# Optimization experiments

Measured on AMD Instinct MI355X. Metric: run time of the kernel, lower is better.

Reference implementation:

```python
import jax, jax.numpy as jnp
import numpy as np

B, T, H = 2048, 64, 64
N_LANE, N_PHASE = 8, 8
# phase -> (lane1, lane2) from phase_startLane_mapping (lanes indexed 0..7)
PHASE_LANES = np.array([[1, 3], [0, 2], [5, 7], [4, 6], [0, 1], [2, 3], [4, 5], [6, 7]])
# pairwise (i, j) with i != j, row-major i then j (matches the python double loop)
I_IDX = np.repeat(np.arange(N_PHASE), N_PHASE - 1).reshape(N_PHASE, N_PHASE - 1)
J_IDX = np.array([[j for j in range(N_PHASE) if j != i] for i in range(N_PHASE)])
# per-lane history gather: [idx, idx+phase_dim, idx+phase_dim+vehicle_dim]
HIST_IDX = np.stack([np.arange(N_LANE), np.arange(N_LANE) + 8, np.arange(N_LANE) + 16], axis=-1)


def setup_inputs():
    key = jax.random.key(0)
    ks = jax.random.split(key, 16)
    ph_bits = jax.random.randint(ks[0], (B, 8), 0, 2).astype(jnp.float32)
    veh_cnt = jax.random.uniform(ks[1], (B, 8)) * 10.0
    feature_input = jnp.concatenate([ph_bits, veh_cnt], axis=-1)  # [B,16]
    history_input = jax.random.uniform(ks[2], (B, T, 24))
    relation = jax.random.randint(ks[3], (8, 7), 0, 2).astype(jnp.int32)
    s = 0.2
    p = {}
    p['emb_phase'] = jax.random.normal(ks[4], (2, 4)) * s
    p['Wv'] = jax.random.normal(ks[5], (4, 1)) * s
    p['bv'] = jnp.zeros((4,))
    p['Wh'] = jax.random.normal(ks[6], (4, 3)) * s
    p['bh'] = jnp.zeros((4,))
    p['Wih'] = jax.random.normal(ks[7], (3 * H, 4)) * s
    p['Whh'] = jax.random.normal(ks[8], (3 * H, H)) * s
    p['bih'] = jnp.zeros((3 * H,))
    p['bhh'] = jnp.zeros((3 * H,))
    p['Wl'] = jax.random.normal(ks[9], (16, 8 + H)) * s
    p['bl'] = jnp.zeros((16,))
    p['emb_const'] = jax.random.normal(ks[10], (2, 4)) * s
    p['Wcf'] = jax.random.normal(ks[11], (20, 32)) * s
    p['bcf'] = jnp.zeros((20,))
    p['Wcc'] = jax.random.normal(ks[12], (20, 4)) * s
    p['bcc'] = jnp.zeros((20,))
    p['Wcm'] = jax.random.normal(ks[13], (20, 20)) * s
    p['bcm'] = jnp.zeros((20,))
    p['Wfin'] = jax.random.normal(ks[14], (1, 20)) * s
    p['bfin'] = jnp.zeros((1,))
    return {'feature_input': feature_input, 'history_input': history_input, 'relation': relation, **p}


def _gru_last(x, Wih, Whh, bih, bhh):
    # x: [N, T, 4] -> final hidden state [N, H]; PyTorch GRU gate order (r, z, n)
    n = x.shape[0]
    h_dim = Whh.shape[1]

    def step(hprev, xt):
        gi = xt @ Wih.T + bih          # [N, 3H]
        gh = hprev @ Whh.T + bhh       # [N, 3H]
        i_r, i_z, i_n = jnp.split(gi, 3, axis=-1)
        h_r, h_z, h_n = jnp.split(gh, 3, axis=-1)
        r = jax.nn.sigmoid(i_r + h_r)
        z = jax.nn.sigmoid(i_z + h_z)
        cand = jnp.tanh(i_n + r * h_n)
        hnew = (1 - z) * cand + z * hprev
        return hnew, None

    h0 = jnp.zeros((n, h_dim), x.dtype)
    hT, _ = jax.lax.scan(step, h0, jnp.swapaxes(x, 0, 1))
    return hT


def _forward(feature_input, history_input, relation, emb_phase, Wv, bv, Wh, bh,
             Wih, Whh, bih, bhh, Wl, bl, emb_const, Wcf, bcf, Wcc, bcc, Wcm, bcm, Wfin, bfin):
    b = feature_input.shape[0]
    phase_ids = jax.lax.stop_gradient(feature_input[:, :8]).astype(jnp.int32)
    veh_raw = feature_input[:, 8:]                                     # [B,8]
    ph = jax.nn.sigmoid(emb_phase[phase_ids])                          # [B,8,4]
    veh = jax.nn.sigmoid(veh_raw[..., None] * Wv[:, 0] + bv)           # Linear(1,4): [B,8,4]
    hist = history_input[:, :, HIST_IDX]                               # [B,T,8,3]
    hist = jax.nn.sigmoid(jnp.einsum('btlc,oc->btlo', hist, Wh) + bh)  # [B,T,8,4]
    x = jnp.swapaxes(hist, 1, 2).reshape(b * N_LANE, T, 4)
    hidden = _gru_last(x, Wih, Whh, bih, bhh).reshape(b, N_LANE, H)
    lane_feat = jnp.concatenate([veh, ph, hidden], axis=-1)            # [B,8,8+H]
    line = jax.nn.relu(lane_feat @ Wl.T + bl)                          # [B,8,16]
    pp = line[:, PHASE_LANES].sum(axis=2)                              # phase pressure [B,8,16]
    fm = jnp.concatenate([pp[:, I_IDX], pp[:, J_IDX]], axis=-1)        # [B,8,7,32]
    ce = emb_const[relation]                                           # [8,7,4]
    xf = jax.nn.relu(jnp.einsum('bpqc,oc->bpqo', fm, Wcf) + bcf)       # 1x1 conv [B,8,7,20]
    yc = jax.nn.relu(ce @ Wcc.T + bcc)                                 # [8,7,20] (broadcast over B)
    z = jax.nn.relu(jnp.einsum('bpqc,oc->bpqo', xf * yc, Wcm) + bcm)
    z = jnp.einsum('bpqc,oc->bpqo', z, Wfin) + bfin                    # [B,8,7,1]
    return z.sum(axis=2)[..., 0]                                       # sum over competing phases -> [B,8]


def reference(feature_input, history_input, relation, emb_phase, Wv, bv, Wh, bh,
              Wih, Whh, bih, bhh, Wl, bl, emb_const, Wcf, bcf, Wcc, bcc, Wcm, bcm, Wfin, bfin):
    return _forward(feature_input, history_input, relation, emb_phase, Wv, bv, Wh, bh,
                    Wih, Whh, bih, bhh, Wl, bl, emb_const, Wcf, bcf, Wcc, bcc, Wcm, bcm, Wfin, bfin)
```

## Files before the change

### kernel.cpp

```cpp
#include <hip/hip_runtime.h>

typedef unsigned short u16;
typedef unsigned int   u32;

typedef __attribute__((ext_vector_type(8))) short short8;
typedef __attribute__((ext_vector_type(4))) float f32x4;

union Frag { u32 u[4]; short8 s; };

__device__ __forceinline__ u32 fbits(float f){ union{float f;u32 u;}x; x.f=f; return x.u; }
__device__ __forceinline__ float bitsf(u32 u){ union{u32 u;float f;}x; x.u=u; return x.f; }
__device__ __forceinline__ u32 pack_trunc(float a, float b){
    return __builtin_amdgcn_perm(fbits(b), fbits(a), 0x07060302u);
}
__device__ __forceinline__ u32 bf16_rne(float a){
    u32 u = fbits(a); return (u + 0x7FFFu + ((u >> 16) & 1u)) >> 16;
}
__device__ __forceinline__ u32 pack_rne(float a, float b){
    return bf16_rne(a) | (bf16_rne(b) << 16);
}
__device__ __forceinline__ float sigmoidf_(float x){
    return __builtin_amdgcn_rcpf(1.0f + __expf(-x));
}

#define LOG2E 1.4426950408889634f

struct __align__(16) SharedMem {
    union {
        struct {
            u16 hh[2][16][72];
            u16 hl[2][16][72];
            u32 uallp[64][16][4];
        } lp;
        struct {
            float wl[1152];
            float bl[16];
            float wcf[640];
            float bcf[20];
            float wcc[80];
            float bcc[20];
            float wcm[400];
            float bcm[20];
            float wfin[20];
            float bfin;
            float line[2][128];
            float pp[2][128];
        } tl;
    };
    float h[16 * 68];
};

__global__ __launch_bounds__(256, 4)
void FRAPRQ_fused_kernel(
    const float* __restrict__ feat,
    const float* __restrict__ hist,
    const int*   __restrict__ relation,
    const float* __restrict__ emb_phase,
    const float* __restrict__ Wv,
    const float* __restrict__ bv,
    const float* __restrict__ Wh,
    const float* __restrict__ bh,
    const float* __restrict__ Wih,
    const float* __restrict__ Whh,
    const float* __restrict__ bih,
    const float* __restrict__ bhh,
    const float* __restrict__ Wl,
    const float* __restrict__ bl,
    const float* __restrict__ emb_const,
    const float* __restrict__ Wcf,
    const float* __restrict__ bcf,
    const float* __restrict__ Wcc,
    const float* __restrict__ bcc,
    const float* __restrict__ Wcm,
    const float* __restrict__ bcm,
    const float* __restrict__ Wfin,
    const float* __restrict__ bfin,
    float* __restrict__ out)
{
    __shared__ SharedMem sm;
    const int tid  = threadIdx.x;
    const int w    = tid >> 6;
    const int lane = tid & 63;
    const int sq   = lane & 15;
    const int q    = lane >> 4;
    const int b_base = blockIdx.x * 2;

    {
        u32* z = (u32*)&sm.lp.hh[0][0][0];
        #pragma unroll 1
        for (int i = tid; i < 2304; i += 256) z[i] = 0u;
    }

    {
        const int s  = tid & 15;
        const int tg = tid >> 4;
        const int bs_ = b_base + (s >> 3), ls_ = s & 7;
        const float* hbp = hist + (size_t)bs_ * 1536;
        float whc[12], bhc[4];
        #pragma unroll
        for (int c = 0; c < 4; ++c){
            whc[c*3+0] = Wh[c*3+0]; whc[c*3+1] = Wh[c*3+1]; whc[c*3+2] = Wh[c*3+2];
            bhc[c] = bh[c];
        }
        #pragma unroll
        for (int i = 0; i < 4; ++i){
            const int t = tg * 4 + i;
            const float x0 = hbp[t*24 + ls_];
            const float x1 = hbp[t*24 + ls_ + 8];
            const float x2 = hbp[t*24 + ls_ + 16];
            float u_[4];
            #pragma unroll
            for (int c = 0; c < 4; ++c)
                u_[c] = sigmoidf_(fmaf(whc[c*3], x0, fmaf(whc[c*3+1], x1, fmaf(whc[c*3+2], x2, bhc[c]))));
            const u32 uh01 = pack_rne(u_[0], u_[1]);
            const u32 uh23 = pack_rne(u_[2], u_[3]);
            const float l0 = u_[0] - bitsf((uh01 & 0xFFFFu) << 16);
            const float l1 = u_[1] - bitsf(uh01 & 0xFFFF0000u);
            const float l2 = u_[2] - bitsf((uh23 & 0xFFFFu) << 16);
            const float l3 = u_[3] - bitsf(uh23 & 0xFFFF0000u);
            *(uint4*)&sm.lp.uallp[t][s][0] =
                make_uint4(uh01, uh23, pack_rne(l0, l1), pack_rne(l2, l3));
        }
    }

    const float gsc[3] = { -LOG2E, -LOG2E, 2.0f * LOG2E };

    Frag ahi[6], alo[6];
    #pragma unroll
    for (int g3 = 0; g3 < 3; ++g3){
        #pragma unroll
        for (int c = 0; c < 2; ++c){
            const int idx = g3 * 2 + c;
            const float* wp = Whh + (64 * g3 + 16 * w + sq) * 64 + 32 * c + 8 * q;
            const float4 fA = *(const float4*)wp;
            const float4 fB = *(const float4*)(wp + 4);
            const float s3 = gsc[g3];
            const float f[8] = {fA.x*s3, fA.y*s3, fA.z*s3, fA.w*s3,
                                fB.x*s3, fB.y*s3, fB.z*s3, fB.w*s3};
            #pragma unroll
            for (int p = 0; p < 4; ++p){
                const u32 hi = pack_rne(f[2*p], f[2*p+1]);
                ahi[idx].u[p] = hi;
                const float l0 = f[2*p]   - bitsf((hi & 0xFFFFu) << 16);
                const float l1 = f[2*p+1] - bitsf(hi & 0xFFFF0000u);
                alo[idx].u[p] = pack_rne(l0, l1);
            }
        }
    }

    Frag auR, auZ, auN;
    {
        Frag* dst[3] = { &auR, &auZ, &auN };
        #pragma unroll
        for (int g3 = 0; g3 < 3; ++g3){
            const int row = 64 * g3 + 16 * w + sq;
            const float4 wv4 = *(const float4*)&Wih[row * 4];
            const float s3 = gsc[g3];
            const float v0 = wv4.x*s3, v1 = wv4.y*s3, v2 = wv4.z*s3, v3 = wv4.w*s3;
            const u32 whi01 = pack_rne(v0, v1);
            const u32 whi23 = pack_rne(v2, v3);
            const float r0 = v0 - bitsf((whi01 & 0xFFFFu) << 16);
            const float r1 = v1 - bitsf(whi01 & 0xFFFF0000u);
            const float r2 = v2 - bitsf((whi23 & 0xFFFFu) << 16);
            const float r3 = v3 - bitsf(whi23 & 0xFFFF0000u);
            const u32 wlo01 = pack_rne(r0, r1);
            const u32 wlo23 = pack_rne(r2, r3);
            dst[g3]->u[0] = (q <= 1) ? whi01 : 0u;
            dst[g3]->u[1] = (q <= 1) ? whi23 : 0u;
            dst[g3]->u[2] = (q == 0) ? wlo01 : 0u;
            dst[g3]->u[3] = (q == 0) ? wlo23 : 0u;
        }
    }

    f32x4 bR4, bZ4, bNh4, bNi4;
    #pragma unroll
    for (int r = 0; r < 4; ++r){
        const int j = 16 * w + 4 * q + r;
        bR4[r]  = -LOG2E * (bih[j]       + bhh[j]);
        bZ4[r]  = -LOG2E * (bih[64 + j]  + bhh[64 + j]);
        bNi4[r] = 2.0f * LOG2E * bih[128 + j];
        bNh4[r] = 2.0f * LOG2E * bhh[128 + j];
    }

    float hreg[4] = {0.f, 0.f, 0.f, 0.f};

    __syncthreads();

    #define MFMA_(A,B,C) __builtin_amdgcn_mfma_f32_16x16x32_bf16(A, B, C, 0, 0, 0)

    #pragma unroll 1
    for (int t = 0; t < 64; ++t){
        const int rb = t & 1;

        const short8 bh0 = *(const short8*)&sm.lp.hh[rb][sq][8 * q];
        const short8 bl0 = *(const short8*)&sm.lp.hl[rb][sq][8 * q];
        const short8 bh1 = *(const short8*)&sm.lp.hh[rb][sq][32 + 8 * q];
        const short8 bl1 = *(const short8*)&sm.lp.hl[rb][sq][32 + 8 * q];
        const uint4 uv = *(const uint4*)&sm.lp.uallp[t][sq][0];
        Frag bu;
        bu.u[0] = (q == 0) ? uv.x : ((q == 1) ? uv.z : 0u);
        bu.u[1] = (q == 0) ? uv.y : ((q == 1) ? uv.w : 0u);
        bu.u[2] = (q == 0) ? uv.x : 0u;
        bu.u[3] = (q == 0) ? uv.y : 0u;

        f32x4 aR = MFMA_(auR.s, bu.s, bR4);
        aR = MFMA_(ahi[0].s, bh0, aR); aR = MFMA_(ahi[0].s, bl0, aR); aR = MFMA_(alo[0].s, bh0, aR);
        aR = MFMA_(ahi[1].s, bh1, aR); aR = MFMA_(ahi[1].s, bl1, aR); aR = MFMA_(alo[1].s, bh1, aR);
        f32x4 aZ = MFMA_(auZ.s, bu.s, bZ4);
        aZ = MFMA_(ahi[2].s, bh0, aZ); aZ = MFMA_(ahi[2].s, bl0, aZ); aZ = MFMA_(alo[2].s, bh0, aZ);
        aZ = MFMA_(ahi[3].s, bh1, aZ); aZ = MFMA_(ahi[3].s, bl1, aZ); aZ = MFMA_(alo[3].s, bh1, aZ);
        f32x4 aN = MFMA_(ahi[4].s, bh0, bNh4);
        aN = MFMA_(ahi[4].s, bl0, aN); aN = MFMA_(alo[4].s, bh0, aN);
        aN = MFMA_(ahi[5].s, bh1, aN); aN = MFMA_(ahi[5].s, bl1, aN); aN = MFMA_(alo[5].s, bh1, aN);
        f32x4 gN = MFMA_(auN.s, bu.s, bNi4);

        float hn4[4];
        #pragma unroll
        for (int r = 0; r < 4; ++r){
            const float rr   = __builtin_amdgcn_rcpf(1.0f + __builtin_amdgcn_exp2f(aR[r]));
            const float zz   = __builtin_amdgcn_rcpf(1.0f + __builtin_amdgcn_exp2f(aZ[r]));
            const float y    = fmaf(rr, aN[r], gN[r]);
            const float cand = fmaf(-2.0f,
                __builtin_amdgcn_rcpf(__builtin_amdgcn_exp2f(y) + 1.0f), 1.0f);
            const float hn   = fmaf(zz, hreg[r] - cand, cand);
            hreg[r] = hn;
            hn4[r] = hn;
        }

        {
            const u32 hi0 = pack_trunc(hn4[0], hn4[1]);
            const u32 hi1 = pack_trunc(hn4[2], hn4[3]);
            const float l0 = hn4[0] - bitsf((hi0 & 0xFFFFu) << 16);
            const float l1 = hn4[1] - bitsf(hi0 & 0xFFFF0000u);
            const float l2 = hn4[2] - bitsf((hi1 & 0xFFFFu) << 16);
            const float l3 = hn4[3] - bitsf(hi1 & 0xFFFF0000u);
            const u32 lo0 = pack_trunc(l0, l1);
            const u32 lo1 = pack_trunc(l2, l3);
            const int wb = rb ^ 1;
            *(uint2*)&sm.lp.hh[wb][sq][16 * w + 4 * q] = make_uint2(hi0, hi1);
            *(uint2*)&sm.lp.hl[wb][sq][16 * w + 4 * q] = make_uint2(lo0, lo1);
        }

        __syncthreads();
    }
    #undef MFMA_

    {
        const float4 hv = make_float4(hreg[0], hreg[1], hreg[2], hreg[3]);
        *(float4*)&sm.h[sq * 68 + 16 * w + 4 * q] = hv;
    }

    for (int i = tid; i < 1152; i += 256) sm.tl.wl[i]  = Wl[i];
    for (int i = tid; i <  640; i += 256) sm.tl.wcf[i] = Wcf[i];
    for (int i = tid; i <  400; i += 256) sm.tl.wcm[i] = Wcm[i];
    if (tid < 80) sm.tl.wcc[tid] = Wcc[tid];
    if (tid < 20){
        sm.tl.bcf[tid]  = bcf[tid];
        sm.tl.bcc[tid]  = bcc[tid];
        sm.tl.bcm[tid]  = bcm[tid];
        sm.tl.wfin[tid] = Wfin[tid];
    }
    if (tid < 16) sm.tl.bl[tid] = bl[tid];
    if (tid == 0) sm.tl.bfin = bfin[0];
    __syncthreads();

    {
        const int g    = w & 1;
        const int half = w >> 1;
        const int b    = b_base + g;
        const int l = lane >> 3, o = lane & 7;
        float fv[8];
        const float vraw = feat[b * 16 + 8 + l];
        const int   bit  = ((int)feat[b * 16 + l]) & 1;
        #pragma unroll
        for (int c = 0; c < 4; ++c){
            fv[c]     = sigmoidf_(fmaf(vraw, Wv[c], bv[c]));
            fv[4 + c] = sigmoidf_(emb_phase[bit * 4 + c]);
        }
        const float* hrow = &sm.h[(g * 8 + l) * 68];
        const int oo = o + half * 8;
        float acc = sm.tl.bl[oo];
        #pragma unroll
        for (int f = 0; f < 8; ++f) acc = fmaf(fv[f], sm.tl.wl[oo * 72 + f], acc);
        for (int k = 0; k < 64; ++k) acc = fmaf(hrow[k], sm.tl.wl[oo * 72 + 8 + k], acc);
        sm.tl.line[g][l * 16 + oo] = fmaxf(acc, 0.0f);
    }
    __syncthreads();

    if (w < 2){
        const int g = w;
        const int b = b_base + g;
        {
            const int p = lane >> 3, o = lane & 7;
            const int l0 = (0x64204501u >> (p * 4)) & 15;
            const int l1 = (0x75316723u >> (p * 4)) & 15;
            sm.tl.pp[g][p * 16 + o]     = sm.tl.line[g][l0 * 16 + o]     + sm.tl.line[g][l1 * 16 + o];
            sm.tl.pp[g][p * 16 + o + 8] = sm.tl.line[g][l0 * 16 + o + 8] + sm.tl.line[g][l1 * 16 + o + 8];
        }
        __builtin_amdgcn_wave_barrier();
        if (lane < 56){
            const int p  = lane / 7;
            const int qi = lane - p * 7;
            const int jl = qi + (qi >= p ? 1 : 0);
            float fmv[32];
            #pragma unroll
            for (int f = 0; f < 16; ++f){
                fmv[f]      = sm.tl.pp[g][p  * 16 + f];
                fmv[16 + f] = sm.tl.pp[g][jl * 16 + f];
            }
            const int rel = relation[p * 7 + qi] & 1;
            float ce[4];
            #pragma unroll
            for (int c = 0; c < 4; ++c) ce[c] = emb_const[rel * 4 + c];
            float m[20];
            for (int o = 0; o < 20; ++o){
                float xf = sm.tl.bcf[o];
                #pragma unroll
                for (int f = 0; f < 32; ++f) xf = fmaf(fmv[f], sm.tl.wcf[o * 32 + f], xf);
                float yc = sm.tl.bcc[o];
                #pragma unroll
                for (int c = 0; c < 4; ++c) yc = fmaf(ce[c], sm.tl.wcc[o * 4 + c], yc);
                m[o] = fmaxf(xf, 0.0f) * fmaxf(yc, 0.0f);
            }
            float fin = sm.tl.bfin;
            for (int o = 0; o < 20; ++o){
                float zz = sm.tl.bcm[o];
                #pragma unroll
                for (int c = 0; c < 20; ++c) zz = fmaf(m[c], sm.tl.wcm[o * 20 + c], zz);
                fin = fmaf(fmaxf(zz, 0.0f), sm.tl.wfin[o], fin);
            }
            sm.tl.line[g][lane] = fin;
        }
        __builtin_amdgcn_wave_barrier();
        if (lane < 8){
            float acc = 0.0f;
            #pragma unroll
            for (int qq = 0; qq < 7; ++qq) acc += sm.tl.line[g][lane * 7 + qq];
            out[b * 8 + lane] = acc;
        }
    }
}

extern "C" void kernel_launch(void* const* d_in, const int* in_sizes, int n_in,
                              void* d_out, int out_size, void* d_ws, size_t ws_size,
                              hipStream_t stream) {
    (void)n_in; (void)d_ws; (void)ws_size; (void)out_size;
    const float* feat      = (const float*)d_in[0];
    const float* hist      = (const float*)d_in[1];
    const int*   relation  = (const int*)d_in[2];
    const float* emb_phase = (const float*)d_in[3];
    const float* Wv        = (const float*)d_in[4];
    const float* bv        = (const float*)d_in[5];
    const float* Wh        = (const float*)d_in[6];
    const float* bh        = (const float*)d_in[7];
    const float* Wih       = (const float*)d_in[8];
    const float* Whh       = (const float*)d_in[9];
    const float* bih       = (const float*)d_in[10];
    const float* bhh       = (const float*)d_in[11];
    const float* Wl        = (const float*)d_in[12];
    const float* bl        = (const float*)d_in[13];
    const float* emb_const = (const float*)d_in[14];
    const float* Wcf       = (const float*)d_in[15];
    const float* bcf       = (const float*)d_in[16];
    const float* Wcc       = (const float*)d_in[17];
    const float* bcc       = (const float*)d_in[18];
    const float* Wcm       = (const float*)d_in[19];
    const float* bcm       = (const float*)d_in[20];
    const float* Wfin      = (const float*)d_in[21];
    const float* bfin      = (const float*)d_in[22];
    float* out = (float*)d_out;

    const int B = in_sizes[0] / 16;
    const int nblocks = B / 2;
    FRAPRQ_fused_kernel<<<nblocks, 256, 0, stream>>>(
        feat, hist, relation, emb_phase, Wv, bv, Wh, bh, Wih, Whh, bih, bhh,
        Wl, bl, emb_const, Wcf, bcf, Wcc, bcc, Wcm, bcm, Wfin, bfin, out);
}
```

Measured before the change: 200.1 us.

## Process two independent 16-sequence GRU tiles per block to share weights and barriers

Each block now handles 4 batch items (two 16-row GRU tiles) instead of 2, reusing the register-resident Whh fragments for both tiles and interleaving two independent MFMA chains per timestep. This amortizes the per-step __syncthreads and the weight setup, and gives the scheduler independent work to hide MFMA and transcendental latency. The tail stage is restructured so each wave handles one batch item end to end. In exchange, LDS per block roughly doubles, launch bounds drop to 2 blocks per CU, and the grid halves, which reduces occupancy.

Measured after the change: 204.7 us. +2.3%, slower.

```diff
diff --git a/kernel.cpp b/kernel.cpp
--- a/kernel.cpp
+++ b/kernel.cpp
@@ -28,9 +28,9 @@
 struct __align__(16) SharedMem {
     union {
         struct {
-            u16 hh[2][16][72];
-            u16 hl[2][16][72];
-            u32 uallp[64][16][4];
+            u16 hh[2][2][16][72];
+            u16 hl[2][2][16][72];
+            u32 uallp[2][64][16][4];
         } lp;
         struct {
             float wl[1152];
@@ -43,14 +43,14 @@
             float bcm[20];
             float wfin[20];
             float bfin;
-            float line[2][128];
-            float pp[2][128];
+            float line[4][128];
+            float pp[4][128];
         } tl;
     };
-    float h[16 * 68];
+    float h[32 * 68];
 };
 
-__global__ __launch_bounds__(256, 4)
+__global__ __launch_bounds__(256, 2)
 void FRAPRQ_fused_kernel(
     const float* __restrict__ feat,
     const float* __restrict__ hist,
@@ -83,18 +83,19 @@
     const int lane = tid & 63;
     const int sq   = lane & 15;
     const int q    = lane >> 4;
-    const int b_base = blockIdx.x * 2;
+    const int b_base = blockIdx.x * 4;
 
     {
-        u32* z = (u32*)&sm.lp.hh[0][0][0];
+        u32* z = (u32*)&sm.lp.hh[0][0][0][0];
         #pragma unroll 1
-        for (int i = tid; i < 2304; i += 256) z[i] = 0u;
+        for (int i = tid; i < 4608; i += 256) z[i] = 0u;
     }
 
     {
         const int s  = tid & 15;
-        const int tg = tid >> 4;
-        const int bs_ = b_base + (s >> 3), ls_ = s & 7;
+        const int pr = (tid >> 4) & 1;
+        const int tg = tid >> 5;
+        const int bs_ = b_base + pr * 2 + (s >> 3), ls_ = s & 7;
         const float* hbp = hist + (size_t)bs_ * 1536;
         float whc[12], bhc[4];
         #pragma unroll
@@ -103,8 +104,8 @@
             bhc[c] = bh[c];
         }
         #pragma unroll
-        for (int i = 0; i < 4; ++i){
-            const int t = tg * 4 + i;
+        for (int i = 0; i < 8; ++i){
+            const int t = tg * 8 + i;
             const float x0 = hbp[t*24 + ls_];
             const float x1 = hbp[t*24 + ls_ + 8];
             const float x2 = hbp[t*24 + ls_ + 16];
@@ -118,7 +119,7 @@
             const float l1 = u_[1] - bitsf(uh01 & 0xFFFF0000u);
             const float l2 = u_[2] - bitsf((uh23 & 0xFFFFu) << 16);
             const float l3 = u_[3] - bitsf(uh23 & 0xFFFF0000u);
-            *(uint4*)&sm.lp.uallp[t][s][0] =
+            *(uint4*)&sm.lp.uallp[pr][t][s][0] =
                 make_uint4(uh01, uh23, pack_rne(l0, l1), pack_rne(l2, l3));
         }
     }
@@ -182,7 +183,7 @@
         bNh4[r] = 2.0f * LOG2E * bhh[128 + j];
     }
 
-    float hreg[4] = {0.f, 0.f, 0.f, 0.f};
+    float hreg[2][4] = {{0.f,0.f,0.f,0.f},{0.f,0.f,0.f,0.f}};
 
     __syncthreads();
 
@@ -192,42 +193,47 @@
     for (int t = 0; t < 64; ++t){
         const int rb = t & 1;
 
-        const short8 bh0 = *(const short8*)&sm.lp.hh[rb][sq][8 * q];
-        const short8 bl0 = *(const short8*)&sm.lp.hl[rb][sq][8 * q];
-        const short8 bh1 = *(const short8*)&sm.lp.hh[rb][sq][32 + 8 * q];
-        const short8 bl1 = *(const short8*)&sm.lp.hl[rb][sq][32 + 8 * q];
-        const uint4 uv = *(const uint4*)&sm.lp.uallp[t][sq][0];
-        Frag bu;
-        bu.u[0] = (q == 0) ? uv.x : ((q == 1) ? uv.z : 0u);
-        bu.u[1] = (q == 0) ? uv.y : ((q == 1) ? uv.w : 0u);
-        bu.u[2] = (q == 0) ? uv.x : 0u;
-        bu.u[3] = (q == 0) ? uv.y : 0u;
-
-        f32x4 aR = MFMA_(auR.s, bu.s, bR4);
-        aR = MFMA_(ahi[0].s, bh0, aR); aR = MFMA_(ahi[0].s, bl0, aR); aR = MFMA_(alo[0].s, bh0, aR);
-        aR = MFMA_(ahi[1].s, bh1, aR); aR = MFMA_(ahi[1].s, bl1, aR); aR = MFMA_(alo[1].s, bh1, aR);
-        f32x4 aZ = MFMA_(auZ.s, bu.s, bZ4);
-        aZ = MFMA_(ahi[2].s, bh0, aZ); aZ = MFMA_(ahi[2].s, bl0, aZ); aZ = MFMA_(alo[2].s, bh0, aZ);
-        aZ = MFMA_(ahi[3].s, bh1, aZ); aZ = MFMA_(ahi[3].s, bl1, aZ); aZ = MFMA_(alo[3].s, bh1, aZ);
-        f32x4 aN = MFMA_(ahi[4].s, bh0, bNh4);
-        aN = MFMA_(ahi[4].s, bl0, aN); aN = MFMA_(alo[4].s, bh0, aN);
-        aN = MFMA_(ahi[5].s, bh1, aN); aN = MFMA_(ahi[5].s, bl1, aN); aN = MFMA_(alo[5].s, bh1, aN);
-        f32x4 gN = MFMA_(auN.s, bu.s, bNi4);
-
-        float hn4[4];
-        #pragma unroll
-        for (int r = 0; r < 4; ++r){
-            const float rr   = __builtin_amdgcn_rcpf(1.0f + __builtin_amdgcn_exp2f(aR[r]));
-            const float zz   = __builtin_amdgcn_rcpf(1.0f + __builtin_amdgcn_exp2f(aZ[r]));
-            const float y    = fmaf(rr, aN[r], gN[r]);
-            const float cand = fmaf(-2.0f,
-                __builtin_amdgcn_rcpf(__builtin_amdgcn_exp2f(y) + 1.0f), 1.0f);
-            const float hn   = fmaf(zz, hreg[r] - cand, cand);
-            hreg[r] = hn;
-            hn4[r] = hn;
-        }
-
-        {
+        short8 bh0[2], bl0[2], bh1[2], bl1[2];
+        Frag bu[2];
+        #pragma unroll
+        for (int p = 0; p < 2; ++p){
+            bh0[p] = *(const short8*)&sm.lp.hh[p][rb][sq][8 * q];
+            bl0[p] = *(const short8*)&sm.lp.hl[p][rb][sq][8 * q];
+            bh1[p] = *(const short8*)&sm.lp.hh[p][rb][sq][32 + 8 * q];
+            bl1[p] = *(const short8*)&sm.lp.hl[p][rb][sq][32 + 8 * q];
+            const uint4 uv = *(const uint4*)&sm.lp.uallp[p][t][sq][0];
+            bu[p].u[0] = (q == 0) ? uv.x : ((q == 1) ? uv.z : 0u);
+            bu[p].u[1] = (q == 0) ? uv.y : ((q == 1) ? uv.w : 0u);
+            bu[p].u[2] = (q == 0) ? uv.x : 0u;
+            bu[p].u[3] = (q == 0) ? uv.y : 0u;
+        }
+
+        #pragma unroll
+        for (int p = 0; p < 2; ++p){
+            f32x4 aR = MFMA_(auR.s, bu[p].s, bR4);
+            aR = MFMA_(ahi[0].s, bh0[p], aR); aR = MFMA_(ahi[0].s, bl0[p], aR); aR = MFMA_(alo[0].s, bh0[p], aR);
+            aR = MFMA_(ahi[1].s, bh1[p], aR); aR = MFMA_(ahi[1].s, bl1[p], aR); aR = MFMA_(alo[1].s, bh1[p], aR);
+            f32x4 aZ = MFMA_(auZ.s, bu[p].s, bZ4);
+            aZ = MFMA_(ahi[2].s, bh0[p], aZ); aZ = MFMA_(ahi[2].s, bl0[p], aZ); aZ = MFMA_(alo[2].s, bh0[p], aZ);
+            aZ = MFMA_(ahi[3].s, bh1[p], aZ); aZ = MFMA_(ahi[3].s, bl1[p], aZ); aZ = MFMA_(alo[3].s, bh1[p], aZ);
+            f32x4 aN = MFMA_(ahi[4].s, bh0[p], bNh4);
+            aN = MFMA_(ahi[4].s, bl0[p], aN); aN = MFMA_(alo[4].s, bh0[p], aN);
+            aN = MFMA_(ahi[5].s, bh1[p], aN); aN = MFMA_(ahi[5].s, bl1[p], aN); aN = MFMA_(alo[5].s, bh1[p], aN);
+            f32x4 gN = MFMA_(auN.s, bu[p].s, bNi4);
+
+            float hn4[4];
+            #pragma unroll
+            for (int r = 0; r < 4; ++r){
+                const float rr   = __builtin_amdgcn_rcpf(1.0f + __builtin_amdgcn_exp2f(aR[r]));
+                const float zz   = __builtin_amdgcn_rcpf(1.0f + __builtin_amdgcn_exp2f(aZ[r]));
+                const float y    = fmaf(rr, aN[r], gN[r]);
+                const float cand = fmaf(-2.0f,
+                    __builtin_amdgcn_rcpf(__builtin_amdgcn_exp2f(y) + 1.0f), 1.0f);
+                const float hn   = fmaf(zz, hreg[p][r] - cand, cand);
+                hreg[p][r] = hn;
+                hn4[r] = hn;
+            }
+
             const u32 hi0 = pack_trunc(hn4[0], hn4[1]);
             const u32 hi1 = pack_trunc(hn4[2], hn4[3]);
             const float l0 = hn4[0] - bitsf((hi0 & 0xFFFFu) << 16);
@@ -237,17 +243,18 @@
             const u32 lo0 = pack_trunc(l0, l1);
             const u32 lo1 = pack_trunc(l2, l3);
             const int wb = rb ^ 1;
-            *(uint2*)&sm.lp.hh[wb][sq][16 * w + 4 * q] = make_uint2(hi0, hi1);
-            *(uint2*)&sm.lp.hl[wb][sq][16 * w + 4 * q] = make_uint2(lo0, lo1);
+            *(uint2*)&sm.lp.hh[p][wb][sq][16 * w + 4 * q] = make_uint2(hi0, hi1);
+            *(uint2*)&sm.lp.hl[p][wb][sq][16 * w + 4 * q] = make_uint2(lo0, lo1);
         }
 
         __syncthreads();
     }
     #undef MFMA_
 
-    {
-        const float4 hv = make_float4(hreg[0], hreg[1], hreg[2], hreg[3]);
-        *(float4*)&sm.h[sq * 68 + 16 * w + 4 * q] = hv;
+    #pragma unroll
+    for (int p = 0; p < 2; ++p){
+        const float4 hv = make_float4(hreg[p][0], hreg[p][1], hreg[p][2], hreg[p][3]);
+        *(float4*)&sm.h[(p * 16 + sq) * 68 + 16 * w + 4 * q] = hv;
     }
 
     for (int i = tid; i < 1152; i += 256) sm.tl.wl[i]  = Wl[i];
@@ -265,9 +272,7 @@
     __syncthreads();
 
     {
-        const int g    = w & 1;
-        const int half = w >> 1;
-        const int b    = b_base + g;
+        const int b = b_base + w;
         const int l = lane >> 3, o = lane & 7;
         float fv[8];
         const float vraw = feat[b * 16 + 8 + l];
@@ -277,25 +282,23 @@
             fv[c]     = sigmoidf_(fmaf(vraw, Wv[c], bv[c]));
             fv[4 + c] = sigmoidf_(emb_phase[bit * 4 + c]);
         }
-        const float* hrow = &sm.h[(g * 8 + l) * 68];
-        const int oo = o + half * 8;
-        float acc = sm.tl.bl[oo];
-        #pragma unroll
-        for (int f = 0; f < 8; ++f) acc = fmaf(fv[f], sm.tl.wl[oo * 72 + f], acc);
-        for (int k = 0; k < 64; ++k) acc = fmaf(hrow[k], sm.tl.wl[oo * 72 + 8 + k], acc);
-        sm.tl.line[g][l * 16 + oo] = fmaxf(acc, 0.0f);
-    }
-    __syncthreads();
-
-    if (w < 2){
-        const int g = w;
-        const int b = b_base + g;
+        const float* hrow = &sm.h[((w >> 1) * 16 + (w & 1) * 8 + l) * 68];
+        #pragma unroll
+        for (int half = 0; half < 2; ++half){
+            const int oo = o + half * 8;
+            float acc = sm.tl.bl[oo];
+            #pragma unroll
+            for (int f = 0; f < 8; ++f) acc = fmaf(fv[f], sm.tl.wl[oo * 72 + f], acc);
+            for (int k = 0; k < 64; ++k) acc = fmaf(hrow[k], sm.tl.wl[oo * 72 + 8 + k], acc);
+            sm.tl.line[w][l * 16 + oo] = fmaxf(acc, 0.0f);
+        }
+        __builtin_amdgcn_wave_barrier();
         {
-            const int p = lane >> 3, o = lane & 7;
+            const int p = lane >> 3, oo = lane & 7;
             const int l0 = (0x64204501u >> (p * 4)) & 15;
             const int l1 = (0x75316723u >> (p * 4)) & 15;
-            sm.tl.pp[g][p * 16 + o]     = sm.tl.line[g][l0 * 16 + o]     + sm.tl.line[g][l1 * 16 + o];
-            sm.tl.pp[g][p * 16 + o + 8] = sm.tl.line[g][l0 * 16 + o + 8] + sm.tl.line[g][l1 * 16 + o + 8];
+            sm.tl.pp[w][p * 16 + oo]     = sm.tl.line[w][l0 * 16 + oo]     + sm.tl.line[w][l1 * 16 + oo];
+            sm.tl.pp[w][p * 16 + oo + 8] = sm.tl.line[w][l0 * 16 + oo + 8] + sm.tl.line[w][l1 * 16 + oo + 8];
         }
         __builtin_amdgcn_wave_barrier();
         if (lane < 56){
@@ -305,37 +308,37 @@
             float fmv[32];
             #pragma unroll
             for (int f = 0; f < 16; ++f){
-                fmv[f]      = sm.tl.pp[g][p  * 16 + f];
-                fmv[16 + f] = sm.tl.pp[g][jl * 16 + f];
+                fmv[f]      = sm.tl.pp[w][p  * 16 + f];
+                fmv[16 + f] = sm.tl.pp[w][jl * 16 + f];
             }
             const int rel = relation[p * 7 + qi] & 1;
             float ce[4];
             #pragma unroll
             for (int c = 0; c < 4; ++c) ce[c] = emb_const[rel * 4 + c];
             float m[20];
-            for (int o = 0; o < 20; ++o){
-                float xf = sm.tl.bcf[o];
+            for (int o2 = 0; o2 < 20; ++o2){
+                float xf = sm.tl.bcf[o2];
                 #pragma unroll
-                for (int f = 0; f < 32; ++f) xf = fmaf(fmv[f], sm.tl.wcf[o * 32 + f], xf);
-                float yc = sm.tl.bcc[o];
+                for (int f = 0; f < 32; ++f) xf = fmaf(fmv[f], sm.tl.wcf[o2 * 32 + f], xf);
+                float yc = sm.tl.bcc[o2];
                 #pragma unroll
-                for (int c = 0; c < 4; ++c) yc = fmaf(ce[c], sm.tl.wcc[o * 4 + c], yc);
-                m[o] = fmaxf(xf, 0.0f) * fmaxf(yc, 0.0f);
+                for (int c = 0; c < 4; ++c) yc = fmaf(ce[c], sm.tl.wcc[o2 * 4 + c], yc);
+                m[o2] = fmaxf(xf, 0.0f) * fmaxf(yc, 0.0f);
             }
             float fin = sm.tl.bfin;
-            for (int o = 0; o < 20; ++o){
-                float zz = sm.tl.bcm[o];
+            for (int o2 = 0; o2 < 20; ++o2){
+                float zz = sm.tl.bcm[o2];
                 #pragma unroll
-                for (int c = 0; c < 20; ++c) zz = fmaf(m[c], sm.tl.wcm[o * 20 + c], zz);
-                fin = fmaf(fmaxf(zz, 0.0f), sm.tl.wfin[o], fin);
-            }
-            sm.tl.line[g][lane] = fin;
+                for (int c = 0; c < 20; ++c) zz = fmaf(m[c], sm.tl.wcm[o2 * 20 + c], zz);
+                fin = fmaf(fmaxf(zz, 0.0f), sm.tl.wfin[o2], fin);
+            }
+            sm.tl.line[w][lane] = fin;
         }
         __builtin_amdgcn_wave_barrier();
         if (lane < 8){
             float acc = 0.0f;
             #pragma unroll
-            for (int qq = 0; qq < 7; ++qq) acc += sm.tl.line[g][lane * 7 + qq];
+            for (int qq = 0; qq < 7; ++qq) acc += sm.tl.line[w][lane * 7 + qq];
             out[b * 8 + lane] = acc;
         }
     }
@@ -371,7 +374,7 @@
     float* out = (float*)d_out;
 
     const int B = in_sizes[0] / 16;
-    const int nblocks = B / 2;
+    const int nblocks = B / 4;
     FRAPRQ_fused_kernel<<<nblocks, 256, 0, stream>>>(
         feat, hist, relation, emb_phase, Wv, bv, Wh, bh, Wih, Whh, bih, bhh,
         Wl, bl, emb_const, Wcf, bcf, Wcc, bcc, Wcm, bcm, Wfin, bfin, out);
```
